# Kernel tuning notes

Measured on AMD Instinct MI355X. Metric: run time of the kernel, lower is better.

Reference implementation:

```python
import jax, jax.numpy as jnp
import numpy as np

SPATIAL = ((100, 134), (50, 67), (25, 34), (13, 17))
LEN = sum(h * w for h, w in SPATIAL)   # 17821
D, H, L, P = 384, 8, 4, 4
DH = D // H                            # 48
U = D // 3                             # unit_dim = 128
EPS = 1e-5


def _ln(x, g, b):
    m = jnp.mean(x, -1, keepdims=True)
    v = jnp.mean((x - m) ** 2, -1, keepdims=True)
    return (x - m) * jax.lax.rsqrt(v + EPS) * g + b


def _ffn(t, w1, b1, w2, b2, g, b):
    t2 = jax.nn.relu(t @ w1.T + b1) @ w2.T + b2
    return _ln(t + t2, g, b)


def _msda_core(value, loc, attn):
    # value [B,Lv,H,DH]; loc [B,Lq,H,L,P,2] normalized to [0,1]; attn [B,Lq,H,L,P]
    B = value.shape[0]
    Lq = loc.shape[1]
    out = jnp.zeros((B, H, Lq, DH), value.dtype)
    start = 0
    for lvl, (Hl, Wl) in enumerate(SPATIAL):
        n = Hl * Wl
        v = value[:, start:start + n].transpose(0, 2, 1, 3)        # [B,H,n,DH]
        # grid_sample(align_corners=False) semantics: pixel coord = loc*W - 0.5
        x = loc[:, :, :, lvl, :, 0] * Wl - 0.5                      # [B,Lq,H,P]
        y = loc[:, :, :, lvl, :, 1] * Hl - 0.5
        x0 = jnp.floor(x); y0 = jnp.floor(y)
        dx = x - x0; dy = y - y0
        x0i = x0.astype(jnp.int32); y0i = y0.astype(jnp.int32)
        acc = jnp.zeros((B, H, Lq, P, DH), value.dtype)
        corners = ((0, 0, (1 - dx) * (1 - dy)), (1, 0, dx * (1 - dy)),
                   (0, 1, (1 - dx) * dy), (1, 1, dx * dy))
        for ox, oy, w in corners:
            xi = x0i + ox; yi = y0i + oy
            valid = ((xi >= 0) & (xi < Wl) & (yi >= 0) & (yi < Hl)).astype(value.dtype)
            idx = jnp.clip(yi, 0, Hl - 1) * Wl + jnp.clip(xi, 0, Wl - 1)
            idx_t = idx.transpose(0, 2, 1, 3).reshape(B, H, Lq * P)
            g = jnp.take_along_axis(v, idx_t[..., None], axis=2).reshape(B, H, Lq, P, DH)
            acc = acc + g * (w * valid).transpose(0, 2, 1, 3)[..., None]
        out = out + (acc * attn[:, :, :, lvl].transpose(0, 2, 1, 3)[..., None]).sum(axis=3)
        start += n
    return out.transpose(0, 2, 1, 3).reshape(B, Lq, D)


def setup_inputs() -> dict:
    key = jax.random.key(0)
    ks = jax.random.split(key, 16)
    rn = lambda k, s, sc=1.0: jax.random.normal(k, s, jnp.float32) * sc
    inp = {}
    inp['src'] = rn(ks[0], (1, LEN, D))
    inp['space_query'] = rn(ks[1], (1, 1, 2 * U))
    inp['chann_query'] = rn(ks[2], (1, 1, 2 * U))
    inp['pos'] = rn(ks[3], (1, LEN, D))
    inp['reference_points'] = jax.random.uniform(ks[4], (1, LEN, L, 2), jnp.float32)
    inp['spatial_shapes'] = jnp.array(SPATIAL, jnp.int32)
    starts = np.cumsum([0] + [h * w for h, w in SPATIAL[:-1]])
    inp['level_start_index'] = jnp.array(starts, jnp.int32)
    inp['padding_mask'] = jnp.zeros((1, LEN), bool)
    # MSDeformAttn params (torch Linear convention: W is [out_features, in_features])
    inp['W_off'] = rn(ks[5], (H * L * P * 2, D), 0.01)
    inp['b_off'] = rn(ks[6], (H * L * P * 2,), 0.1)
    inp['W_attn'] = rn(ks[7], (H * L * P, D), D ** -0.5)
    inp['b_attn'] = jnp.zeros((H * L * P,), jnp.float32)
    inp['W_val'] = rn(ks[8], (D, D), D ** -0.5)
    inp['b_val'] = jnp.zeros((D,), jnp.float32)
    inp['W_out'] = rn(ks[9], (D, D), D ** -0.5)
    inp['b_out'] = jnp.zeros((D,), jnp.float32)
    # norm1_xy / norm1_zd
    inp['g1xy'] = jnp.ones((2 * U,), jnp.float32); inp['b1xy'] = jnp.zeros((2 * U,), jnp.float32)
    inp['g1zd'] = jnp.ones((U,), jnp.float32); inp['b1zd'] = jnp.zeros((U,), jnp.float32)
    # ffn_xy: Linear(2U,2U) -> relu -> Linear(2U,2U), residual + LN
    inp['fxy_w1'] = rn(ks[10], (2 * U, 2 * U), (2 * U) ** -0.5); inp['fxy_b1'] = jnp.zeros((2 * U,), jnp.float32)
    inp['fxy_w2'] = rn(ks[11], (2 * U, 2 * U), (2 * U) ** -0.5); inp['fxy_b2'] = jnp.zeros((2 * U,), jnp.float32)
    inp['fxy_g'] = jnp.ones((2 * U,), jnp.float32); inp['fxy_b'] = jnp.zeros((2 * U,), jnp.float32)
    # ffn_zd: Linear(U,U) -> relu -> Linear(U,U), residual + LN
    inp['fzd_w1'] = rn(ks[12], (U, U), U ** -0.5); inp['fzd_b1'] = jnp.zeros((U,), jnp.float32)
    inp['fzd_w2'] = rn(ks[13], (U, U), U ** -0.5); inp['fzd_b2'] = jnp.zeros((U,), jnp.float32)
    inp['fzd_g'] = jnp.ones((U,), jnp.float32); inp['fzd_b'] = jnp.zeros((U,), jnp.float32)
    return inp


def reference(src, space_query, chann_query, pos, reference_points, spatial_shapes,
              level_start_index, padding_mask,
              W_off, b_off, W_attn, b_attn, W_val, b_val, W_out, b_out,
              g1xy, b1xy, g1zd, b1zd,
              fxy_w1, fxy_b1, fxy_w2, fxy_b2, fxy_g, fxy_b,
              fzd_w1, fzd_b1, fzd_w2, fzd_b2, fzd_g, fzd_b):
    B, Lq, _ = src.shape
    q = src + pos                                        # with_pos_embed
    value = src @ W_val.T + b_val
    value = jnp.where(padding_mask[..., None], 0.0, value).reshape(B, Lq, H, DH)
    off = (q @ W_off.T + b_off).reshape(B, Lq, H, L, P, 2)
    attn = jax.nn.softmax((q @ W_attn.T + b_attn).reshape(B, Lq, H, L * P), -1)
    attn = attn.reshape(B, Lq, H, L, P)
    wh = jnp.array([[w, h] for h, w in SPATIAL], src.dtype)         # [L,2] as (W,H)
    loc = reference_points[:, :, None, :, None, :] + off / wh[None, None, None, :, None, :]
    src2 = _msda_core(value, loc, attn) @ W_out.T + b_out
    src_xy = _ln(src[..., :2 * U] + src2[..., :2 * U], g1xy, b1xy)
    src_zd = _ln(src[..., 2 * U:] + src2[..., 2 * U:], g1zd, b1zd)
    src_xy = _ffn(src_xy, fxy_w1, fxy_b1, fxy_w2, fxy_b2, fxy_g, fxy_b)
    src_zd = _ffn(src_zd, fzd_w1, fzd_b1, fzd_w2, fzd_b2, fzd_g, fzd_b)
    return jnp.concatenate([src_xy, src_zd], axis=-1)
```

## Files before the change

### kernel.cpp

```cpp
#include <hip/hip_runtime.h>
#include <math.h>

#define LEN 17821
#define DMODEL 384
#define NHEAD 8
#define DHEAD 48
#define WSZ (384 * 384)

typedef float floatx4 __attribute__((ext_vector_type(4)));
typedef float floatx2 __attribute__((ext_vector_type(2)));
typedef short shortx8 __attribute__((ext_vector_type(8)));
typedef unsigned short ushort;

__device__ inline ushort f2bf(float f) {
    unsigned int u = __float_as_uint(f);
    u += 0x7FFFu + ((u >> 16) & 1u);
    return (ushort)(u >> 16);
}
__device__ inline float bf2f(ushort s) {
    return __uint_as_float(((unsigned int)s) << 16);
}

__device__ inline floatx4 mfma_bf16(shortx8 a, shortx8 b, floatx4 c) {
    return __builtin_amdgcn_mfma_f32_16x16x32_bf16(a, b, c, 0, 0, 0);
}

__global__ __launch_bounds__(256)
void prep_w(const float* __restrict__ Wval, const float* __restrict__ Woff,
            const float* __restrict__ Wattn, const float* __restrict__ Wout,
            const float* __restrict__ w1xy, const float* __restrict__ w1zd,
            const float* __restrict__ w2xy, const float* __restrict__ w2zd,
            ushort* __restrict__ wv, ushort* __restrict__ woa,
            ushort* __restrict__ wo, ushort* __restrict__ w1b,
            ushort* __restrict__ w2b) {
    int idx = blockIdx.x * 256 + threadIdx.x;
    if (idx >= WSZ) return;
    int job = blockIdx.y;
    int e = idx & 7;
    int lane = (idx >> 3) & 63;
    int t = idx >> 9;
    int j = t % 3;
    int t2 = t / 3;
    int wv8 = t2 & 7;
    int hs = t2 >> 3;
    int l15 = lane & 15, quad = lane >> 4;
    int row = wv8 * 48 + j * 16 + l15;
    int k = hs * 32 + quad * 8 + e;
    float v; ushort* dst;
    if (job == 0) { v = Wval[row * 384 + k]; dst = wv; }
    else if (job == 1) {
        v = row < 256 ? Woff[row * 384 + k] : Wattn[(row - 256) * 384 + k];
        dst = woa;
    } else if (job == 2) { v = Wout[row * 384 + k]; dst = wo; }
    else if (job == 3) {
        v = row < 256 ? (k < 256 ? w1xy[row * 256 + k] : 0.f)
                      : (k >= 256 ? w1zd[(row - 256) * 128 + (k - 256)] : 0.f);
        dst = w1b;
    } else {
        v = row < 256 ? (k < 256 ? w2xy[row * 256 + k] : 0.f)
                      : (k >= 256 ? w2zd[(row - 256) * 128 + (k - 256)] : 0.f);
        dst = w2b;
    }
    dst[idx] = f2bf(v);
}

__global__ __launch_bounds__(384)
void prep_b(const float* __restrict__ boff, const float* __restrict__ battn,
            const float* __restrict__ b1xy, const float* __restrict__ b1zd,
            const float* __restrict__ b2xy, const float* __restrict__ b2zd,
            const float* __restrict__ g1xy, const float* __restrict__ be1xy,
            const float* __restrict__ g1zd, const float* __restrict__ be1zd,
            const float* __restrict__ g2xy, const float* __restrict__ be2xy,
            const float* __restrict__ g2zd, const float* __restrict__ be2zd,
            float* __restrict__ boa, float* __restrict__ b1c,
            float* __restrict__ b2c, float* __restrict__ l1g,
            float* __restrict__ l1b, float* __restrict__ l2g,
            float* __restrict__ l2b) {
    int i = threadIdx.x;
    bool lo = i < 256; int j = lo ? i : i - 256;
    boa[i] = lo ? boff[i] : battn[j];
    b1c[i] = lo ? b1xy[i] : b1zd[j];
    b2c[i] = lo ? b2xy[i] : b2zd[j];
    l1g[i] = lo ? g1xy[i] : g1zd[j];
    l1b[i] = lo ? be1xy[i] : be1zd[j];
    l2g[i] = lo ? g2xy[i] : g2zd[j];
    l2b[i] = lo ? be2xy[i] : be2zd[j];
}

#define MT 32
#define CST 392

#define GEMM384(WPTR)                                                         \
  {                                                                           \
    const ushort* wp_ = (WPTR) + wave * 1536 + lane * 8;                      \
    _Pragma("unroll")                                                         \
    for (int i_ = 0; i_ < 2; ++i_)                                            \
      _Pragma("unroll")                                                       \
      for (int j_ = 0; j_ < 3; ++j_) acc[i_][j_] = (floatx4){0.f,0.f,0.f,0.f};\
    shortx8 wcr[3], wnr[3];                                                   \
    _Pragma("unroll")                                                         \
    for (int j_ = 0; j_ < 3; ++j_)                                            \
      wcr[j_] = *(const shortx8*)(wp_ + j_ * 512);                            \
    _Pragma("unroll")                                                         \
    for (int hs = 0; hs < 12; ++hs) {                                         \
      if (hs < 11) {                                                          \
        _Pragma("unroll")                                                     \
        for (int j_ = 0; j_ < 3; ++j_)                                        \
          wnr[j_] = *(const shortx8*)(wp_ + (hs + 1) * 12288 + j_ * 512);     \
      }                                                                       \
      shortx8 a0 = *(shortx8*)&Cbuf[l15 * CST + hs * 32 + quad * 8];          \
      shortx8 a1 = *(shortx8*)&Cbuf[(16 + l15) * CST + hs * 32 + quad * 8];   \
      _Pragma("unroll")                                                       \
      for (int j_ = 0; j_ < 3; ++j_) {                                        \
        acc[0][j_] = mfma_bf16(a0, wcr[j_], acc[0][j_]);                      \
        acc[1][j_] = mfma_bf16(a1, wcr[j_], acc[1][j_]);                      \
      }                                                                       \
      if (hs < 11) {                                                          \
        _Pragma("unroll")                                                     \
        for (int j_ = 0; j_ < 3; ++j_) wcr[j_] = wnr[j_];                     \
      }                                                                       \
    }                                                                         \
  }

__global__ __launch_bounds__(512, 2)
void vq_gemm(const float* __restrict__ src, const float* __restrict__ pos,
             const ushort* __restrict__ wv, const ushort* __restrict__ woa,
             const float* __restrict__ bval, const float* __restrict__ boa,
             ushort* __restrict__ vout, float* __restrict__ oaout) {
    __shared__ __align__(16) ushort Cbuf[MT * CST];
    bool job = blockIdx.y != 0;
    const ushort* Wp = job ? woa : wv;
    const float* bias = job ? boa : bval;
    int tid = threadIdx.x;
    int lane = tid & 63, wave = tid >> 6;
    int l15 = lane & 15, quad = lane >> 4;
    int wcol = wave * 48;
    int by0 = blockIdx.x * MT;

    #pragma unroll
    for (int cix = 0; cix < 3; ++cix) {
        int idx = cix * 512 + tid;
        int row = idx / 48, c = idx - row * 48;
        int gr = min(by0 + row, LEN - 1);
        const float* sp = src + (size_t)gr * 384 + c * 8;
        float4 a0 = *(const float4*)sp, a1 = *(const float4*)(sp + 4);
        if (job) {
            const float* pp = pos + (size_t)gr * 384 + c * 8;
            float4 p0 = *(const float4*)pp, p1 = *(const float4*)(pp + 4);
            a0.x += p0.x; a0.y += p0.y; a0.z += p0.z; a0.w += p0.w;
            a1.x += p1.x; a1.y += p1.y; a1.z += p1.z; a1.w += p1.w;
        }
        shortx8 b;
        b[0] = f2bf(a0.x); b[1] = f2bf(a0.y); b[2] = f2bf(a0.z); b[3] = f2bf(a0.w);
        b[4] = f2bf(a1.x); b[5] = f2bf(a1.y); b[6] = f2bf(a1.z); b[7] = f2bf(a1.w);
        *(shortx8*)(Cbuf + row * CST + c * 8) = b;
    }
    __syncthreads();

    floatx4 acc[2][3];
    GEMM384(Wp);

    #pragma unroll
    for (int j = 0; j < 3; ++j) {
        int col = wcol + j * 16 + l15;
        float bv = bias[col];
        #pragma unroll
        for (int i = 0; i < 2; ++i) {
            #pragma unroll
            for (int rr = 0; rr < 4; ++rr) {
                int gr = by0 + i * 16 + quad * 4 + rr;
                if (gr < LEN) {
                    float v = acc[i][j][rr] + bv;
                    if (job) oaout[(size_t)gr * 384 + col] = v;
                    else     vout[(size_t)gr * 384 + col] = f2bf(v);
                }
            }
        }
    }
}

#define MTOK 8
#define NXCD 8
__global__ __launch_bounds__(384)
void msda_v4(const ushort* __restrict__ value,
             const float* __restrict__ offattn,
             const float* __restrict__ refpts,
             ushort* __restrict__ out, int nwg) {
    __shared__ float saw[MTOK * 128];
    __shared__ int   si4[MTOK * 128][4];
    __shared__ float sw4[MTOK * 128][4];
    constexpr int Wi[4]  = {134, 67, 34, 17};
    constexpr int Hi[4]  = {100, 50, 25, 13};
    constexpr int STi[4] = {0, 13400, 16750, 17600};

    int orig = blockIdx.x;
    int q = nwg / NXCD, r = nwg % NXCD;
    int xcd = orig % NXCD, ci = orig / NXCD;
    int bid = (xcd < r ? xcd * (q + 1) : r * (q + 1) + (xcd - r) * q) + ci;
    int t0 = bid * MTOK;
    int tid = threadIdx.x;

    if (tid < MTOK * 8) {
        int ti = tid >> 3, h = tid & 7, t = t0 + ti;
        if (t < LEN) {
            const float* lg = offattn + (size_t)t * 384 + 256 + h * 16;
            float w[16], mx = -3.4e38f;
            #pragma unroll
            for (int s = 0; s < 16; ++s) { w[s] = lg[s]; mx = fmaxf(mx, w[s]); }
            float sum = 0.f;
            #pragma unroll
            for (int s = 0; s < 16; ++s) { w[s] = __expf(w[s] - mx); sum += w[s]; }
            float inv = 1.0f / sum;
            #pragma unroll
            for (int s = 0; s < 16; ++s) saw[ti * 128 + h * 16 + s] = w[s] * inv;
        }
    }
    __syncthreads();

    for (int idx = tid; idx < MTOK * 128; idx += 384) {
        int ti = idx >> 7, rem = idx & 127, h = rem >> 4, p = rem & 15;
        int lvl = p >> 2, pp = p & 3;
        int t = t0 + ti;
        if (t < LEN) {
            float Wl = (float)Wi[lvl], Hl = (float)Hi[lvl];
            const int Wli = Wi[lvl], Hli = Hi[lvl], st = STi[lvl];
            const float* op = offattn + (size_t)t * 384 + h * 32 + lvl * 8 + pp * 2;
            float ox = op[0], oy = op[1];
            float rx = refpts[(size_t)t * 8 + lvl * 2];
            float ry = refpts[(size_t)t * 8 + lvl * 2 + 1];
            float x = rx * Wl + ox - 0.5f;
            float y = ry * Hl + oy - 0.5f;
            float x0f = floorf(x), y0f = floorf(y);
            int x0 = (int)x0f, y0 = (int)y0f;
            float dx = x - x0f, dy = y - y0f;
            float aw = saw[idx];
            float cwv[4] = {(1.f - dx) * (1.f - dy), dx * (1.f - dy),
                            (1.f - dx) * dy, dx * dy};
            #pragma unroll
            for (int c2 = 0; c2 < 4; ++c2) {
                int xi = x0 + (c2 & 1), yi = y0 + (c2 >> 1);
                bool valid = (xi >= 0) & (xi < Wli) & (yi >= 0) & (yi < Hli);
                int xc = min(max(xi, 0), Wli - 1);
                int yc = min(max(yi, 0), Hli - 1);
                si4[idx][c2] = st + yc * Wli + xc;
                sw4[idx][c2] = valid ? aw * cwv[c2] : 0.f;
            }
        }
    }
    __syncthreads();

    int ti = tid / 48;
    int rr = tid - ti * 48;
    int h = rr / 6;
    int c = rr - h * 6;
    int t = t0 + ti;
    if (t >= LEN) return;
    const ushort* vb = value + h * DHEAD + c * 8;
    floatx2 a2[4] = {};
    #pragma unroll
    for (int p = 0; p < 16; ++p) {
        int base = ti * 128 + h * 16 + p;
        int4  I = *(const int4*)&si4[base][0];
        float4 W4 = *(const float4*)&sw4[base][0];
        const int   Iv[4] = {I.x, I.y, I.z, I.w};
        const float Wv[4] = {W4.x, W4.y, W4.z, W4.w};
        #pragma unroll
        for (int c2 = 0; c2 < 4; ++c2) {
            shortx8 g = *(const shortx8*)(vb + (size_t)Iv[c2] * 384);
            float s = Wv[c2];
            floatx2 s2 = {s, s};
            const unsigned int* gu = (const unsigned int*)&g;
            #pragma unroll
            for (int q2 = 0; q2 < 4; ++q2) {
                unsigned int u = gu[q2];
                floatx2 gf;
                gf[0] = __uint_as_float(u << 16);
                gf[1] = __uint_as_float(u & 0xFFFF0000u);
                a2[q2] += s2 * gf;
            }
        }
    }
    shortx8 o;
    #pragma unroll
    for (int q2 = 0; q2 < 4; ++q2) {
        o[q2 * 2]     = f2bf(a2[q2][0]);
        o[q2 * 2 + 1] = f2bf(a2[q2][1]);
    }
    *(shortx8*)(out + (size_t)t * 384 + h * DHEAD + c * 8) = o;
}

__global__ __launch_bounds__(512, 2)
void mega_kernel(const ushort* __restrict__ Amsda, const float* __restrict__ src,
                 const ushort* __restrict__ Wo, const ushort* __restrict__ W1,
                 const ushort* __restrict__ W2,
                 const float* __restrict__ bo, const float* __restrict__ b1c,
                 const float* __restrict__ b2c,
                 const float* __restrict__ l1g, const float* __restrict__ l1b,
                 const float* __restrict__ l2g, const float* __restrict__ l2b,
                 float* __restrict__ h1f, float* __restrict__ outp) {
    __shared__ __align__(16) ushort Cbuf[MT * CST];
    __shared__ __align__(16) floatx4 pst4[MT * 16];
    __shared__ __align__(16) floatx4 lnf[MT];

    int tid = threadIdx.x;
    int lane = tid & 63, wave = tid >> 6;
    int l15 = lane & 15, quad = lane >> 4;
    int wcol = wave * 48;
    int by0 = blockIdx.x * MT;

    floatx4 acc[2][3];

    #pragma unroll
    for (int cix = 0; cix < 3; ++cix) {
        int idx = cix * 512 + tid;
        int row = idx / 48, c = idx - row * 48;
        int gr = min(by0 + row, LEN - 1);
        *(shortx8*)(Cbuf + row * CST + c * 8) =
            *(const shortx8*)(Amsda + (size_t)gr * 384 + c * 8);
    }
    __syncthreads();

    GEMM384(Wo);
    __syncthreads();

    #pragma unroll
    for (int j = 0; j < 3; ++j) {
        int col = wcol + j * 16 + l15;
        float bv = bo[col];
        #pragma unroll
        for (int i = 0; i < 2; ++i)
            #pragma unroll
            for (int rr = 0; rr < 4; ++rr) {
                int row = i * 16 + quad * 4 + rr;
                int gr = min(by0 + row, LEN - 1);
                float x = acc[i][j][rr] + bv + src[(size_t)gr * 384 + col];
                Cbuf[row * CST + col] = f2bf(x);
            }
    }
    __syncthreads();

    {
        int row = tid >> 4, part = tid & 15;
        float sx = 0.f, qx = 0.f, sz = 0.f, qz = 0.f;
        #pragma unroll
        for (int m = 0; m < 3; ++m) {
            int c0 = part * 24 + m * 8;
            shortx8 v = *(shortx8*)(Cbuf + row * CST + c0);
            float cs = 0.f, cq = 0.f;
            #pragma unroll
            for (int e = 0; e < 8; ++e) { float x = bf2f(v[e]); cs += x; cq += x * x; }
            if (c0 < 256) { sx += cs; qx += cq; } else { sz += cs; qz += cq; }
        }
        pst4[row * 16 + part] = (floatx4){sx, qx, sz, qz};
    }
    __syncthreads();
    if (tid < MT) {
        floatx4 s = (floatx4){0.f, 0.f, 0.f, 0.f};
        #pragma unroll
        for (int p = 0; p < 16; ++p) s += pst4[tid * 16 + p];
        float mx = s[0] / 256.f, vx = s[1] / 256.f - mx * mx;
        float mz = s[2] / 128.f, vz = s[3] / 128.f - mz * mz;
        lnf[tid] = (floatx4){mx, rsqrtf(vx + 1e-5f), mz, rsqrtf(vz + 1e-5f)};
    }
    __syncthreads();
    {
        int row = tid >> 4, part = tid & 15;
        int gr = by0 + row;
        floatx4 L = lnf[row];
        #pragma unroll
        for (int m = 0; m < 3; ++m) {
            int c0 = part * 24 + m * 8;
            bool isxy = c0 < 256;
            float mean = isxy ? L[0] : L[2];
            float inv  = isxy ? L[1] : L[3];
            shortx8 v = *(shortx8*)(Cbuf + row * CST + c0);
            float4 g0 = *(const float4*)(l1g + c0), g1 = *(const float4*)(l1g + c0 + 4);
            float4 e0 = *(const float4*)(l1b + c0), e1 = *(const float4*)(l1b + c0 + 4);
            float gg[8] = {g0.x, g0.y, g0.z, g0.w, g1.x, g1.y, g1.z, g1.w};
            float ee[8] = {e0.x, e0.y, e0.z, e0.w, e1.x, e1.y, e1.z, e1.w};
            float h[8];
            shortx8 hb;
            #pragma unroll
            for (int e = 0; e < 8; ++e) {
                h[e] = (bf2f(v[e]) - mean) * inv * gg[e] + ee[e];
                hb[e] = f2bf(h[e]);
            }
            *(shortx8*)(Cbuf + row * CST + c0) = hb;
            if (gr < LEN) {
                *(float4*)(h1f + (size_t)gr * 384 + c0)     = make_float4(h[0], h[1], h[2], h[3]);
                *(float4*)(h1f + (size_t)gr * 384 + c0 + 4) = make_float4(h[4], h[5], h[6], h[7]);
            }
        }
    }
    __syncthreads();

    GEMM384(W1);
    __syncthreads();
    #pragma unroll
    for (int j = 0; j < 3; ++j) {
        int col = wcol + j * 16 + l15;
        float bv = b1c[col];
        #pragma unroll
        for (int i = 0; i < 2; ++i)
            #pragma unroll
            for (int rr = 0; rr < 4; ++rr) {
                int row = i * 16 + quad * 4 + rr;
                Cbuf[row * CST + col] = f2bf(fmaxf(acc[i][j][rr] + bv, 0.f));
            }
    }
    __syncthreads();

    GEMM384(W2);
    __syncthreads();
    #pragma unroll
    for (int j = 0; j < 3; ++j) {
        int col = wcol + j * 16 + l15;
        float bv = b2c[col];
        #pragma unroll
        for (int i = 0; i < 2; ++i)
            #pragma unroll
            for (int rr = 0; rr < 4; ++rr) {
                int row = i * 16 + quad * 4 + rr;
                int gr = min(by0 + row, LEN - 1);
                float x = acc[i][j][rr] + bv + h1f[(size_t)gr * 384 + col];
                Cbuf[row * CST + col] = f2bf(x);
            }
    }
    __syncthreads();

    {
        int row = tid >> 4, part = tid & 15;
        float sx = 0.f, qx = 0.f, sz = 0.f, qz = 0.f;
        #pragma unroll
        for (int m = 0; m < 3; ++m) {
            int c0 = part * 24 + m * 8;
            shortx8 v = *(shortx8*)(Cbuf + row * CST + c0);
            float cs = 0.f, cq = 0.f;
            #pragma unroll
            for (int e = 0; e < 8; ++e) { float x = bf2f(v[e]); cs += x; cq += x * x; }
            if (c0 < 256) { sx += cs; qx += cq; } else { sz += cs; qz += cq; }
        }
        pst4[row * 16 + part] = (floatx4){sx, qx, sz, qz};
    }
    __syncthreads();
    if (tid < MT) {
        floatx4 s = (floatx4){0.f, 0.f, 0.f, 0.f};
        #pragma unroll
        for (int p = 0; p < 16; ++p) s += pst4[tid * 16 + p];
        float mx = s[0] / 256.f, vx = s[1] / 256.f - mx * mx;
        float mz = s[2] / 128.f, vz = s[3] / 128.f - mz * mz;
        lnf[tid] = (floatx4){mx, rsqrtf(vx + 1e-5f), mz, rsqrtf(vz + 1e-5f)};
    }
    __syncthreads();
    {
        int row = tid >> 4, part = tid & 15;
        int gr = by0 + row;
        if (gr < LEN) {
            floatx4 L = lnf[row];
            #pragma unroll
            for (int m = 0; m < 3; ++m) {
                int c0 = part * 24 + m * 8;
                bool isxy = c0 < 256;
                float mean = isxy ? L[0] : L[2];
                float inv  = isxy ? L[1] : L[3];
                shortx8 v = *(shortx8*)(Cbuf + row * CST + c0);
                float4 g0 = *(const float4*)(l2g + c0), g1 = *(const float4*)(l2g + c0 + 4);
                float4 e0 = *(const float4*)(l2b + c0), e1 = *(const float4*)(l2b + c0 + 4);
                float gg[8] = {g0.x, g0.y, g0.z, g0.w, g1.x, g1.y, g1.z, g1.w};
                float ee[8] = {e0.x, e0.y, e0.z, e0.w, e1.x, e1.y, e1.z, e1.w};
                float h[8];
                #pragma unroll
                for (int e = 0; e < 8; ++e)
                    h[e] = (bf2f(v[e]) - mean) * inv * gg[e] + ee[e];
                *(float4*)(outp + (size_t)gr * 384 + c0)     = make_float4(h[0], h[1], h[2], h[3]);
                *(float4*)(outp + (size_t)gr * 384 + c0 + 4) = make_float4(h[4], h[5], h[6], h[7]);
            }
        }
    }
}

extern "C" void kernel_launch(void* const* d_in, const int* in_sizes, int n_in,
                              void* d_out, int out_size, void* d_ws, size_t ws_size,
                              hipStream_t stream) {
    const float* src    = (const float*)d_in[0];
    const float* pos    = (const float*)d_in[3];
    const float* refpts = (const float*)d_in[4];
    const float* W_off  = (const float*)d_in[8];
    const float* b_off  = (const float*)d_in[9];
    const float* W_attn = (const float*)d_in[10];
    const float* b_attn = (const float*)d_in[11];
    const float* W_val  = (const float*)d_in[12];
    const float* b_val  = (const float*)d_in[13];
    const float* W_out  = (const float*)d_in[14];
    const float* b_out  = (const float*)d_in[15];
    const float* g1xy = (const float*)d_in[16]; const float* b1xy = (const float*)d_in[17];
    const float* g1zd = (const float*)d_in[18]; const float* b1zd = (const float*)d_in[19];
    const float* fxy_w1 = (const float*)d_in[20]; const float* fxy_b1 = (const float*)d_in[21];
    const float* fxy_w2 = (const float*)d_in[22]; const float* fxy_b2 = (const float*)d_in[23];
    const float* fxy_g  = (const float*)d_in[24]; const float* fxy_b  = (const float*)d_in[25];
    const float* fzd_w1 = (const float*)d_in[26]; const float* fzd_b1 = (const float*)d_in[27];
    const float* fzd_w2 = (const float*)d_in[28]; const float* fzd_b2 = (const float*)d_in[29];
    const float* fzd_g  = (const float*)d_in[30]; const float* fzd_b  = (const float*)d_in[31];

    float* out = (float*)d_out;
    size_t Rn = (size_t)LEN * DMODEL;

    float* f0 = (float*)d_ws;
    ushort* sb = (ushort*)(f0 + Rn);
    ushort* s2 = sb + 2 * Rn;
    ushort* s3 = sb + 3 * Rn;
    ushort* wv  = sb + 4 * Rn;
    ushort* woa = wv + WSZ;
    ushort* wo  = woa + WSZ;
    ushort* w1b = wo + WSZ;
    ushort* w2b = w1b + WSZ;
    float* bp = (float*)(w2b + WSZ);
    float* boa = bp;        float* b1c = bp + 384;  float* b2c = bp + 768;
    float* l1g = bp + 1152; float* l1b = bp + 1536;
    float* l2g = bp + 1920; float* l2b = bp + 2304;

    prep_w<<<dim3((WSZ + 255) / 256, 5), 256, 0, stream>>>(
        W_val, W_off, W_attn, W_out, fxy_w1, fzd_w1, fxy_w2, fzd_w2,
        wv, woa, wo, w1b, w2b);
    prep_b<<<1, 384, 0, stream>>>(b_off, b_attn, fxy_b1, fzd_b1, fxy_b2, fzd_b2,
                                  g1xy, b1xy, g1zd, b1zd, fxy_g, fxy_b, fzd_g, fzd_b,
                                  boa, b1c, b2c, l1g, l1b, l2g, l2b);

    vq_gemm<<<dim3((LEN + MT - 1) / MT, 2), 512, 0, stream>>>(
        src, pos, wv, woa, b_val, boa, s2, f0);

    int nwg = (LEN + MTOK - 1) / MTOK;
    msda_v4<<<nwg, 384, 0, stream>>>(s2, f0, refpts, s3, nwg);

    mega_kernel<<<(LEN + MT - 1) / MT, 512, 0, stream>>>(
        s3, src, wo, w1b, w2b, b_out, b1c, b2c,
        l1g, l1b, l2g, l2b, f0, out);
}
```

Measured before the change: 296.2 us.

## Fuse MSDA sampling into the output-projection/FFN mega kernel

New measurement: 330.3 us. +11.5%, slower.

```diff
diff --git a/kernel.cpp b/kernel.cpp
--- a/kernel.cpp
+++ b/kernel.cpp
@@ -179,128 +179,30 @@
     }
 }
 
-#define MTOK 8
-#define NXCD 8
-__global__ __launch_bounds__(384)
-void msda_v4(const ushort* __restrict__ value,
-             const float* __restrict__ offattn,
-             const float* __restrict__ refpts,
-             ushort* __restrict__ out, int nwg) {
-    __shared__ float saw[MTOK * 128];
-    __shared__ int   si4[MTOK * 128][4];
-    __shared__ float sw4[MTOK * 128][4];
+#define GTOK 8
+__global__ __launch_bounds__(512, 2)
+void mega_fused(const ushort* __restrict__ value,
+                const float* offattn,
+                const float* __restrict__ refpts,
+                const float* __restrict__ src,
+                const ushort* __restrict__ Wo, const ushort* __restrict__ W1,
+                const ushort* __restrict__ W2,
+                const float* __restrict__ bo, const float* __restrict__ b1c,
+                const float* __restrict__ b2c,
+                const float* __restrict__ l1g, const float* __restrict__ l1b,
+                const float* __restrict__ l2g, const float* __restrict__ l2b,
+                float* h1f,
+                float* __restrict__ outp) {
+    __shared__ __align__(16) ushort Cbuf[MT * CST];
+    __shared__ __align__(16) floatx4 pst4[MT * 16];
+    __shared__ __align__(16) floatx4 lnf[MT];
+    __shared__ float saw[GTOK * 128];
+    __shared__ int   si4[GTOK * 128][4];
+    __shared__ float sw4[GTOK * 128][4];
+
     constexpr int Wi[4]  = {134, 67, 34, 17};
     constexpr int Hi[4]  = {100, 50, 25, 13};
     constexpr int STi[4] = {0, 13400, 16750, 17600};
-
-    int orig = blockIdx.x;
-    int q = nwg / NXCD, r = nwg % NXCD;
-    int xcd = orig % NXCD, ci = orig / NXCD;
-    int bid = (xcd < r ? xcd * (q + 1) : r * (q + 1) + (xcd - r) * q) + ci;
-    int t0 = bid * MTOK;
-    int tid = threadIdx.x;
-
-    if (tid < MTOK * 8) {
-        int ti = tid >> 3, h = tid & 7, t = t0 + ti;
-        if (t < LEN) {
-            const float* lg = offattn + (size_t)t * 384 + 256 + h * 16;
-            float w[16], mx = -3.4e38f;
-            #pragma unroll
-            for (int s = 0; s < 16; ++s) { w[s] = lg[s]; mx = fmaxf(mx, w[s]); }
-            float sum = 0.f;
-            #pragma unroll
-            for (int s = 0; s < 16; ++s) { w[s] = __expf(w[s] - mx); sum += w[s]; }
-            float inv = 1.0f / sum;
-            #pragma unroll
-            for (int s = 0; s < 16; ++s) saw[ti * 128 + h * 16 + s] = w[s] * inv;
-        }
-    }
-    __syncthreads();
-
-    for (int idx = tid; idx < MTOK * 128; idx += 384) {
-        int ti = idx >> 7, rem = idx & 127, h = rem >> 4, p = rem & 15;
-        int lvl = p >> 2, pp = p & 3;
-        int t = t0 + ti;
-        if (t < LEN) {
-            float Wl = (float)Wi[lvl], Hl = (float)Hi[lvl];
-            const int Wli = Wi[lvl], Hli = Hi[lvl], st = STi[lvl];
-            const float* op = offattn + (size_t)t * 384 + h * 32 + lvl * 8 + pp * 2;
-            float ox = op[0], oy = op[1];
-            float rx = refpts[(size_t)t * 8 + lvl * 2];
-            float ry = refpts[(size_t)t * 8 + lvl * 2 + 1];
-            float x = rx * Wl + ox - 0.5f;
-            float y = ry * Hl + oy - 0.5f;
-            float x0f = floorf(x), y0f = floorf(y);
-            int x0 = (int)x0f, y0 = (int)y0f;
-            float dx = x - x0f, dy = y - y0f;
-            float aw = saw[idx];
-            float cwv[4] = {(1.f - dx) * (1.f - dy), dx * (1.f - dy),
-                            (1.f - dx) * dy, dx * dy};
-            #pragma unroll
-            for (int c2 = 0; c2 < 4; ++c2) {
-                int xi = x0 + (c2 & 1), yi = y0 + (c2 >> 1);
-                bool valid = (xi >= 0) & (xi < Wli) & (yi >= 0) & (yi < Hli);
-                int xc = min(max(xi, 0), Wli - 1);
-                int yc = min(max(yi, 0), Hli - 1);
-                si4[idx][c2] = st + yc * Wli + xc;
-                sw4[idx][c2] = valid ? aw * cwv[c2] : 0.f;
-            }
-        }
-    }
-    __syncthreads();
-
-    int ti = tid / 48;
-    int rr = tid - ti * 48;
-    int h = rr / 6;
-    int c = rr - h * 6;
-    int t = t0 + ti;
-    if (t >= LEN) return;
-    const ushort* vb = value + h * DHEAD + c * 8;
-    floatx2 a2[4] = {};
-    #pragma unroll
-    for (int p = 0; p < 16; ++p) {
-        int base = ti * 128 + h * 16 + p;
-        int4  I = *(const int4*)&si4[base][0];
-        float4 W4 = *(const float4*)&sw4[base][0];
-        const int   Iv[4] = {I.x, I.y, I.z, I.w};
-        const float Wv[4] = {W4.x, W4.y, W4.z, W4.w};
-        #pragma unroll
-        for (int c2 = 0; c2 < 4; ++c2) {
-            shortx8 g = *(const shortx8*)(vb + (size_t)Iv[c2] * 384);
-            float s = Wv[c2];
-            floatx2 s2 = {s, s};
-            const unsigned int* gu = (const unsigned int*)&g;
-            #pragma unroll
-            for (int q2 = 0; q2 < 4; ++q2) {
-                unsigned int u = gu[q2];
-                floatx2 gf;
-                gf[0] = __uint_as_float(u << 16);
-                gf[1] = __uint_as_float(u & 0xFFFF0000u);
-                a2[q2] += s2 * gf;
-            }
-        }
-    }
-    shortx8 o;
-    #pragma unroll
-    for (int q2 = 0; q2 < 4; ++q2) {
-        o[q2 * 2]     = f2bf(a2[q2][0]);
-        o[q2 * 2 + 1] = f2bf(a2[q2][1]);
-    }
-    *(shortx8*)(out + (size_t)t * 384 + h * DHEAD + c * 8) = o;
-}
-
-__global__ __launch_bounds__(512, 2)
-void mega_kernel(const ushort* __restrict__ Amsda, const float* __restrict__ src,
-                 const ushort* __restrict__ Wo, const ushort* __restrict__ W1,
-                 const ushort* __restrict__ W2,
-                 const float* __restrict__ bo, const float* __restrict__ b1c,
-                 const float* __restrict__ b2c,
-                 const float* __restrict__ l1g, const float* __restrict__ l1b,
-                 const float* __restrict__ l2g, const float* __restrict__ l2b,
-                 float* __restrict__ h1f, float* __restrict__ outp) {
-    __shared__ __align__(16) ushort Cbuf[MT * CST];
-    __shared__ __align__(16) floatx4 pst4[MT * 16];
-    __shared__ __align__(16) floatx4 lnf[MT];
 
     int tid = threadIdx.x;
     int lane = tid & 63, wave = tid >> 6;
@@ -308,17 +210,101 @@
     int wcol = wave * 48;
     int by0 = blockIdx.x * MT;
 
+    for (int r = 0; r < 4; ++r) {
+        int tb = by0 + r * GTOK;
+        if (tid < GTOK * 8) {
+            int ti = tid >> 3, h = tid & 7, t = tb + ti;
+            if (t < LEN) {
+                const float* lg = offattn + (size_t)t * 384 + 256 + h * 16;
+                float w[16], mx = -3.4e38f;
+                #pragma unroll
+                for (int s = 0; s < 16; ++s) { w[s] = lg[s]; mx = fmaxf(mx, w[s]); }
+                float sum = 0.f;
+                #pragma unroll
+                for (int s = 0; s < 16; ++s) { w[s] = __expf(w[s] - mx); sum += w[s]; }
+                float inv = 1.0f / sum;
+                #pragma unroll
+                for (int s = 0; s < 16; ++s) saw[ti * 128 + h * 16 + s] = w[s] * inv;
+            }
+        }
+        __syncthreads();
+        for (int idx = tid; idx < GTOK * 128; idx += 512) {
+            int ti = idx >> 7, rem = idx & 127, h = rem >> 4, p = rem & 15;
+            int lvl = p >> 2, pp = p & 3;
+            int t = tb + ti;
+            if (t < LEN) {
+                float Wl = (float)Wi[lvl], Hl = (float)Hi[lvl];
+                const int Wli = Wi[lvl], Hli = Hi[lvl], st = STi[lvl];
+                const float* op = offattn + (size_t)t * 384 + h * 32 + lvl * 8 + pp * 2;
+                float ox = op[0], oy = op[1];
+                float rx = refpts[(size_t)t * 8 + lvl * 2];
+                float ry = refpts[(size_t)t * 8 + lvl * 2 + 1];
+                float x = rx * Wl + ox - 0.5f;
+                float y = ry * Hl + oy - 0.5f;
+                float x0f = floorf(x), y0f = floorf(y);
+                int x0 = (int)x0f, y0 = (int)y0f;
+                float dx = x - x0f, dy = y - y0f;
+                float aw = saw[idx];
+                float cwv[4] = {(1.f - dx) * (1.f - dy), dx * (1.f - dy),
+                                (1.f - dx) * dy, dx * dy};
+                #pragma unroll
+                for (int c2 = 0; c2 < 4; ++c2) {
+                    int xi = x0 + (c2 & 1), yi = y0 + (c2 >> 1);
+                    bool valid = (xi >= 0) & (xi < Wli) & (yi >= 0) & (yi < Hli);
+                    int xc = min(max(xi, 0), Wli - 1);
+                    int yc = min(max(yi, 0), Hli - 1);
+                    si4[idx][c2] = st + yc * Wli + xc;
+                    sw4[idx][c2] = valid ? aw * cwv[c2] : 0.f;
+                }
+            }
+        }
+        __syncthreads();
+        if (tid < GTOK * 48) {
+            int ti = tid / 48;
+            int rr2 = tid - ti * 48;
+            int h = rr2 / 6;
+            int c = rr2 - h * 6;
+            int t = tb + ti;
+            int row = r * GTOK + ti;
+            shortx8 o = {};
+            if (t < LEN) {
+                const ushort* vb = value + h * DHEAD + c * 8;
+                floatx2 a2[4] = {};
+                #pragma unroll
+                for (int p = 0; p < 16; ++p) {
+                    int base = ti * 128 + h * 16 + p;
+                    int4  I = *(const int4*)&si4[base][0];
+                    float4 W4 = *(const float4*)&sw4[base][0];
+                    const int   Iv[4] = {I.x, I.y, I.z, I.w};
+                    const float Wv[4] = {W4.x, W4.y, W4.z, W4.w};
+                    #pragma unroll
+                    for (int c2 = 0; c2 < 4; ++c2) {
+                        shortx8 g = *(const shortx8*)(vb + (size_t)Iv[c2] * 384);
+                        float s = Wv[c2];
+                        floatx2 s2 = {s, s};
+                        const unsigned int* gu = (const unsigned int*)&g;
+                        #pragma unroll
+                        for (int q2 = 0; q2 < 4; ++q2) {
+                            unsigned int u = gu[q2];
+                            floatx2 gf;
+                            gf[0] = __uint_as_float(u << 16);
+                            gf[1] = __uint_as_float(u & 0xFFFF0000u);
+                            a2[q2] += s2 * gf;
+                        }
+                    }
+                }
+                #pragma unroll
+                for (int q2 = 0; q2 < 4; ++q2) {
+                    o[q2 * 2]     = f2bf(a2[q2][0]);
+                    o[q2 * 2 + 1] = f2bf(a2[q2][1]);
+                }
+            }
+            *(shortx8*)(Cbuf + row * CST + h * DHEAD + c * 8) = o;
+        }
+        __syncthreads();
+    }
+
     floatx4 acc[2][3];
-
-    #pragma unroll
-    for (int cix = 0; cix < 3; ++cix) {
-        int idx = cix * 512 + tid;
-        int row = idx / 48, c = idx - row * 48;
-        int gr = min(by0 + row, LEN - 1);
-        *(shortx8*)(Cbuf + row * CST + c * 8) =
-            *(const shortx8*)(Amsda + (size_t)gr * 384 + c * 8);
-    }
-    __syncthreads();
 
     GEMM384(Wo);
     __syncthreads();
@@ -508,7 +494,6 @@
     float* f0 = (float*)d_ws;
     ushort* sb = (ushort*)(f0 + Rn);
     ushort* s2 = sb + 2 * Rn;
-    ushort* s3 = sb + 3 * Rn;
     ushort* wv  = sb + 4 * Rn;
     ushort* woa = wv + WSZ;
     ushort* wo  = woa + WSZ;
@@ -529,10 +514,7 @@
     vq_gemm<<<dim3((LEN + MT - 1) / MT, 2), 512, 0, stream>>>(
         src, pos, wv, woa, b_val, boa, s2, f0);
 
-    int nwg = (LEN + MTOK - 1) / MTOK;
-    msda_v4<<<nwg, 384, 0, stream>>>(s2, f0, refpts, s3, nwg);
-
-    mega_kernel<<<(LEN + MT - 1) / MT, 512, 0, stream>>>(
-        s3, src, wo, w1b, w2b, b_out, b1c, b2c,
+    mega_fused<<<(LEN + MT - 1) / MT, 512, 0, stream>>>(
+        s2, f0, refpts, src, wo, w1b, w2b, b_out, b1c, b2c,
         l1g, l1b, l2g, l2b, f0, out);
 }
```
